# Optimization experiments

Hardware: AMD Instinct MI355X
Metric: run time of the kernel (lower is better)

The kernel has to match this reference:

```python
import jax, jax.numpy as jnp
import numpy as np

EMBED_DIM = 1024
NUM_HEADS = 16
HEAD_DIM = EMBED_DIM // NUM_HEADS
B, T_Q, T_K = 2, 2048, 2048


def setup_inputs() -> dict:
    key = jax.random.key(0)
    ks = jax.random.split(key, 11)
    s = 1.0 / np.sqrt(EMBED_DIM)
    return {
        "query": jax.random.normal(ks[0], (B, T_Q, EMBED_DIM), jnp.float32),
        "key": jax.random.normal(ks[1], (B, T_K, EMBED_DIM), jnp.float32),
        "value": jax.random.normal(ks[2], (B, T_K, EMBED_DIM), jnp.float32),
        "Wq": jax.random.normal(ks[3], (EMBED_DIM, EMBED_DIM), jnp.float32) * s,
        "bq": jnp.zeros((EMBED_DIM,), jnp.float32),
        "Wk": jax.random.normal(ks[4], (EMBED_DIM, EMBED_DIM), jnp.float32) * s,
        "bk": jnp.zeros((EMBED_DIM,), jnp.float32),
        "Wv": jax.random.normal(ks[5], (EMBED_DIM, EMBED_DIM), jnp.float32) * s,
        "bv": jnp.zeros((EMBED_DIM,), jnp.float32),
        "Wo": jax.random.normal(ks[6], (EMBED_DIM, EMBED_DIM), jnp.float32) * s,
        "bo": jnp.zeros((EMBED_DIM,), jnp.float32),
    }


def reference(query, key, value, Wq, bq, Wk, bk, Wv, bv, Wo, bo):
    b, tq, _ = query.shape
    tk = key.shape[1]
    # projections -> [B, H, T, Dh]
    q = (query @ Wq.T + bq).reshape(b, tq, NUM_HEADS, HEAD_DIM).transpose(0, 2, 1, 3)
    k = (key @ Wk.T + bk).reshape(b, tk, NUM_HEADS, HEAD_DIM).transpose(0, 2, 1, 3)
    v = (value @ Wv.T + bv).reshape(b, tk, NUM_HEADS, HEAD_DIM).transpose(0, 2, 1, 3)
    scores = jnp.einsum("bhqd,bhkd->bhqk", q, k) / np.sqrt(HEAD_DIM)
    attn = jax.nn.softmax(scores, axis=-1)
    attn = jnp.nan_to_num(attn, nan=0.0)  # matches torch.nan_to_num; dropout is eval-mode identity
    out = jnp.einsum("bhqk,bhkd->bhqd", attn, v)
    out = out.transpose(0, 2, 1, 3).reshape(b, tq, EMBED_DIM)
    return out @ Wo.T + bo
```

## Files before the change

kernel.cpp:

```cpp
#include <hip/hip_runtime.h>
#include <hip/hip_bf16.h>


typedef short bf16x8 __attribute__((ext_vector_type(8)));
typedef short bf16x4 __attribute__((ext_vector_type(4)));
typedef float f32x4 __attribute__((ext_vector_type(4)));

#define B_ 2
#define T_ 2048
#define E_ 1024
#define H_ 16
#define DH_ 64
#define M_ 4096

static __device__ __forceinline__ short f2bf(float f) {
    __hip_bfloat16 h = __float2bfloat16(f);
    return *reinterpret_cast<short*>(&h);
}

static __device__ __forceinline__ bf16x8 cvt8(const float4 a, const float4 b) {
    bf16x8 r;
    r[0] = f2bf(a.x); r[1] = f2bf(a.y); r[2] = f2bf(a.z); r[3] = f2bf(a.w);
    r[4] = f2bf(b.x); r[5] = f2bf(b.y); r[6] = f2bf(b.z); r[7] = f2bf(b.w);
    return r;
}

static __device__ __forceinline__ void async_copy16(const short* g, short* l) {
    __builtin_amdgcn_global_load_lds(
        (const __attribute__((address_space(1))) unsigned int*)g,
        (__attribute__((address_space(3))) unsigned int*)l, 16, 0, 0);
}

__global__ __launch_bounds__(256) void conv_bf16(
    const float* __restrict__ q, const float* __restrict__ k, const float* __restrict__ v,
    const float* __restrict__ wq, const float* __restrict__ wk,
    const float* __restrict__ wv, const float* __restrict__ wo,
    short* __restrict__ qo, short* __restrict__ ko, short* __restrict__ vo,
    short* __restrict__ wqo, short* __restrict__ wko,
    short* __restrict__ wvo, short* __restrict__ woo) {
    const int y = blockIdx.y;
    const float* src; short* dst; int n;
    switch (y) {
        case 0: src = q;  dst = qo;  n = M_ * E_; break;
        case 1: src = k;  dst = ko;  n = M_ * E_; break;
        case 2: src = v;  dst = vo;  n = M_ * E_; break;
        case 3: src = wq; dst = wqo; n = E_ * E_; break;
        case 4: src = wk; dst = wko; n = E_ * E_; break;
        case 5: src = wv; dst = wvo; n = E_ * E_; break;
        default: src = wo; dst = woo; n = E_ * E_; break;
    }
    const int idx = (blockIdx.x * 256 + threadIdx.x) * 8;
    if (idx >= n) return;
    const float4* p = (const float4*)(src + idx);
    *(bf16x8*)(dst + idx) = cvt8(p[0], p[1]);
}

template <int CMODE>
__device__ __forceinline__ void gemm_fast_tile(const short* __restrict__ A,
                                               const short* __restrict__ W,
                                               const float* __restrict__ bias,
                                               void* __restrict__ C, int bx, int by) {
    __shared__ short Asm[128 * 32];
    __shared__ short Wsm[128 * 32];
    const int tid = threadIdx.x;
    const int wave = tid >> 6, lane = tid & 63, quad = lane >> 4, l16 = lane & 15;
    const int wr = wave >> 1, wc = wave & 1;
    const int m_base = by * 128, n_base = bx * 128;

    const int srow = wave * 32 + (lane >> 2);
    const int scol = (lane & 3) * 8;

    f32x4 acc[4][4] = {};

    for (int k0 = 0; k0 < E_; k0 += 32) {
#pragma unroll
        for (int i = 0; i < 2; i++) {
            async_copy16(&A[(size_t)(m_base + srow + i * 16) * E_ + k0 + scol],
                         &Asm[wave * 1024 + i * 512]);
            async_copy16(&W[(size_t)(n_base + srow + i * 16) * E_ + k0 + scol],
                         &Wsm[wave * 1024 + i * 512]);
        }
        __syncthreads();

        bf16x8 af[4], wf[4];
#pragma unroll
        for (int i = 0; i < 4; i++)
            af[i] = *(const bf16x8*)&Asm[(wr * 64 + i * 16 + l16) * 32 + quad * 8];
#pragma unroll
        for (int j = 0; j < 4; j++)
            wf[j] = *(const bf16x8*)&Wsm[(wc * 64 + j * 16 + l16) * 32 + quad * 8];
#pragma unroll
        for (int i = 0; i < 4; i++)
#pragma unroll
            for (int j = 0; j < 4; j++)
                acc[i][j] = __builtin_amdgcn_mfma_f32_16x16x32_bf16(af[i], wf[j], acc[i][j], 0, 0, 0);
        __syncthreads();
    }

    if (CMODE == 2) {
#pragma unroll
        for (int j = 0; j < 4; j++) {
            const int col = n_base + wc * 64 + j * 16 + l16;
            const float bval = bias[col];
            const int h = col >> 6, d = col & 63;
#pragma unroll
            for (int i = 0; i < 4; i++) {
                const int m0 = m_base + wr * 64 + i * 16 + quad * 4;
                const int b = m0 >> 11, t0 = m0 & 2047;
                bf16x4 v;
#pragma unroll
                for (int r = 0; r < 4; r++) v[r] = f2bf(acc[i][j][r] + bval);
                *(bf16x4*)&((short*)C)[((size_t)(b * H_ + h) * DH_ + d) * T_ + t0] = v;
            }
        }
    } else {
#pragma unroll
        for (int j = 0; j < 4; j++) {
            const int col = n_base + wc * 64 + j * 16 + l16;
            const float bval = bias[col];
#pragma unroll
            for (int i = 0; i < 4; i++)
#pragma unroll
                for (int r = 0; r < 4; r++) {
                    const int m = m_base + wr * 64 + i * 16 + quad * 4 + r;
                    const float v = acc[i][j][r] + bval;
                    if (CMODE == 1) ((float*)C)[(size_t)m * E_ + col] = v;
                    else            ((short*)C)[(size_t)m * E_ + col] = f2bf(v);
                }
        }
    }
}

__global__ __launch_bounds__(256) void qkv_gemm_fast(
    const short* __restrict__ q, const short* __restrict__ k, const short* __restrict__ v,
    const short* __restrict__ Wq, const short* __restrict__ Wk, const short* __restrict__ Wv,
    const float* __restrict__ bq, const float* __restrict__ bk, const float* __restrict__ bv,
    short* __restrict__ Qb, short* __restrict__ Kb, short* __restrict__ Vtb) {
    const int z = blockIdx.z;
    if (z == 0)      gemm_fast_tile<0>(q, Wq, bq, Qb,  blockIdx.x, blockIdx.y);
    else if (z == 1) gemm_fast_tile<0>(k, Wk, bk, Kb,  blockIdx.x, blockIdx.y);
    else             gemm_fast_tile<2>(v, Wv, bv, Vtb, blockIdx.x, blockIdx.y);
}

__global__ __launch_bounds__(256) void o_gemm_fast(const short* __restrict__ A,
                                                   const short* __restrict__ W,
                                                   const float* __restrict__ bias,
                                                   float* __restrict__ C) {
    gemm_fast_tile<1>(A, W, bias, C, blockIdx.x, blockIdx.y);
}

template <int A_BF16, int CMODE>
__device__ __forceinline__ void gemm_tile(const void* __restrict__ A,
                                          const float* __restrict__ W,
                                          const float* __restrict__ bias,
                                          void* __restrict__ C, int bx, int by) {
    __shared__ short Alds[128][40];
    __shared__ short Wlds[128][40];
    const int tid = threadIdx.x;
    const int wave = tid >> 6, lane = tid & 63, quad = lane >> 4, l16 = lane & 15;
    const int wr = wave >> 1, wc = wave & 1;
    const int m_base = by * 128, n_base = bx * 128;
    const int srow = tid >> 1, sch = (tid & 1) * 16;

    f32x4 acc[4][4] = {};

    for (int k0 = 0; k0 < E_; k0 += 32) {
        bf16x8 av0, av1, wv0, wv1;
        if (A_BF16) {
            const short* Ab = (const short*)A;
            av0 = *(const bf16x8*)&Ab[(size_t)(m_base + srow) * E_ + k0 + sch];
            av1 = *(const bf16x8*)&Ab[(size_t)(m_base + srow) * E_ + k0 + sch + 8];
        } else {
            const float4* p = (const float4*)((const float*)A +
                              (size_t)(m_base + srow) * E_ + k0 + sch);
            av0 = cvt8(p[0], p[1]);
            av1 = cvt8(p[2], p[3]);
        }
        {
            const float4* p = (const float4*)(W + (size_t)(n_base + srow) * E_ + k0 + sch);
            wv0 = cvt8(p[0], p[1]);
            wv1 = cvt8(p[2], p[3]);
        }
        *(bf16x8*)&Alds[srow][sch]     = av0;
        *(bf16x8*)&Alds[srow][sch + 8] = av1;
        *(bf16x8*)&Wlds[srow][sch]     = wv0;
        *(bf16x8*)&Wlds[srow][sch + 8] = wv1;
        __syncthreads();

        bf16x8 af[4], bfv[4];
#pragma unroll
        for (int i = 0; i < 4; i++)
            af[i] = *(const bf16x8*)&Alds[wr * 64 + i * 16 + l16][quad * 8];
#pragma unroll
        for (int j = 0; j < 4; j++)
            bfv[j] = *(const bf16x8*)&Wlds[wc * 64 + j * 16 + l16][quad * 8];
#pragma unroll
        for (int i = 0; i < 4; i++)
#pragma unroll
            for (int j = 0; j < 4; j++)
                acc[i][j] = __builtin_amdgcn_mfma_f32_16x16x32_bf16(af[i], bfv[j], acc[i][j], 0, 0, 0);
        __syncthreads();
    }

    if (CMODE == 2) {
#pragma unroll
        for (int j = 0; j < 4; j++) {
            const int col = n_base + wc * 64 + j * 16 + l16;
            const float bval = bias[col];
            const int h = col >> 6, d = col & 63;
#pragma unroll
            for (int i = 0; i < 4; i++) {
                const int m0 = m_base + wr * 64 + i * 16 + quad * 4;
                const int b = m0 >> 11, t0 = m0 & 2047;
                bf16x4 v;
#pragma unroll
                for (int r = 0; r < 4; r++) v[r] = f2bf(acc[i][j][r] + bval);
                *(bf16x4*)&((short*)C)[((size_t)(b * H_ + h) * DH_ + d) * T_ + t0] = v;
            }
        }
    } else {
#pragma unroll
        for (int j = 0; j < 4; j++) {
            const int col = n_base + wc * 64 + j * 16 + l16;
            const float bval = bias[col];
#pragma unroll
            for (int i = 0; i < 4; i++)
#pragma unroll
                for (int r = 0; r < 4; r++) {
                    const int m = m_base + wr * 64 + i * 16 + quad * 4 + r;
                    const float v = acc[i][j][r] + bval;
                    if (CMODE == 1) ((float*)C)[(size_t)m * E_ + col] = v;
                    else            ((short*)C)[(size_t)m * E_ + col] = f2bf(v);
                }
        }
    }
}

__global__ __launch_bounds__(256) void qkv_gemm_slow(
    const float* __restrict__ q, const float* __restrict__ k, const float* __restrict__ v,
    const float* __restrict__ Wq, const float* __restrict__ Wk, const float* __restrict__ Wv,
    const float* __restrict__ bq, const float* __restrict__ bk, const float* __restrict__ bv,
    short* __restrict__ Qb, short* __restrict__ Kb, short* __restrict__ Vtb) {
    const int z = blockIdx.z;
    if (z == 0)      gemm_tile<0, 0>(q, Wq, bq, Qb,  blockIdx.x, blockIdx.y);
    else if (z == 1) gemm_tile<0, 0>(k, Wk, bk, Kb,  blockIdx.x, blockIdx.y);
    else             gemm_tile<0, 2>(v, Wv, bv, Vtb, blockIdx.x, blockIdx.y);
}

__global__ __launch_bounds__(256) void o_gemm_slow(const short* __restrict__ A,
                                                   const float* __restrict__ W,
                                                   const float* __restrict__ bias,
                                                   float* __restrict__ C) {
    gemm_tile<1, 1>(A, W, bias, C, blockIdx.x, blockIdx.y);
}

__global__ __launch_bounds__(256) void attn(short* __restrict__ QO,
                                            const short* __restrict__ Kb,
                                            const short* __restrict__ Vtb) {
    __shared__ short Klds[64][72];
    __shared__ short Vl[64][72];
    __shared__ short Pl[4][16][68];

    const int tid = threadIdx.x;
    const int wave = tid >> 6, lane = tid & 63, quad = lane >> 4, l16 = lane & 15;
    const int bh = blockIdx.x;
    const int b = bh >> 4, h = bh & 15;
    const int q0 = blockIdx.y * 64 + wave * 16;
    const size_t base = ((size_t)b * T_) * E_ + (size_t)h * DH_;
    const size_t vbase = (size_t)bh * DH_ * T_;

    bf16x8 qf[2];
    qf[0] = *(const bf16x8*)&QO[base + (size_t)(q0 + l16) * E_ + quad * 8];
    qf[1] = *(const bf16x8*)&QO[base + (size_t)(q0 + l16) * E_ + 32 + quad * 8];

    f32x4 oacc[4] = {};
    float lsum[4] = {0.f, 0.f, 0.f, 0.f};

    const int srow = tid >> 2;
    const int sc = (tid & 3) * 16;

    for (int kt = 0; kt < T_; kt += 64) {
        const size_t krow = base + (size_t)(kt + srow) * E_;
        *(bf16x8*)&Klds[srow][sc]     = *(const bf16x8*)&Kb[krow + sc];
        *(bf16x8*)&Klds[srow][sc + 8] = *(const bf16x8*)&Kb[krow + sc + 8];
        const size_t vrow = vbase + (size_t)srow * T_ + kt;
        *(bf16x8*)&Vl[srow][sc]     = *(const bf16x8*)&Vtb[vrow + sc];
        *(bf16x8*)&Vl[srow][sc + 8] = *(const bf16x8*)&Vtb[vrow + sc + 8];
        __syncthreads();

        f32x4 sacc[4] = {};
#pragma unroll
        for (int ks = 0; ks < 2; ks++)
#pragma unroll
            for (int kn = 0; kn < 4; kn++) {
                bf16x8 kf = *(const bf16x8*)&Klds[kn * 16 + l16][ks * 32 + quad * 8];
                sacc[kn] = __builtin_amdgcn_mfma_f32_16x16x32_bf16(qf[ks], kf, sacc[kn], 0, 0, 0);
            }

#pragma unroll
        for (int r = 0; r < 4; r++) {
            const float p0 = __expf(sacc[0][r] * 0.125f);
            const float p1 = __expf(sacc[1][r] * 0.125f);
            const float p2 = __expf(sacc[2][r] * 0.125f);
            const float p3 = __expf(sacc[3][r] * 0.125f);
            lsum[r] += (p0 + p1) + (p2 + p3);
            short* prow = &Pl[wave][quad * 4 + r][0];
            prow[l16]      = f2bf(p0);
            prow[16 + l16] = f2bf(p1);
            prow[32 + l16] = f2bf(p2);
            prow[48 + l16] = f2bf(p3);
        }
        __syncthreads();

#pragma unroll
        for (int ks = 0; ks < 2; ks++) {
            bf16x8 pf = *(const bf16x8*)&Pl[wave][l16][ks * 32 + quad * 8];
#pragma unroll
            for (int dn = 0; dn < 4; dn++) {
                bf16x8 vf = *(const bf16x8*)&Vl[dn * 16 + l16][ks * 32 + quad * 8];
                oacc[dn] = __builtin_amdgcn_mfma_f32_16x16x32_bf16(pf, vf, oacc[dn], 0, 0, 0);
            }
        }
        __syncthreads();
    }

#pragma unroll
    for (int r = 0; r < 4; r++) {
#pragma unroll
        for (int m = 1; m < 16; m <<= 1) lsum[r] += __shfl_xor(lsum[r], m);
        lsum[r] = 1.0f / lsum[r];
    }

#pragma unroll
    for (int dn = 0; dn < 4; dn++)
#pragma unroll
        for (int r = 0; r < 4; r++) {
            const float v = oacc[dn][r] * lsum[r];
            QO[base + (size_t)(q0 + quad * 4 + r) * E_ + dn * 16 + l16] = f2bf(v);
        }
}

extern "C" void kernel_launch(void* const* d_in, const int* in_sizes, int n_in,
                              void* d_out, int out_size, void* d_ws, size_t ws_size,
                              hipStream_t stream) {
    const float* query = (const float*)d_in[0];
    const float* key   = (const float*)d_in[1];
    const float* value = (const float*)d_in[2];
    const float* Wq = (const float*)d_in[3];
    const float* bq = (const float*)d_in[4];
    const float* Wk = (const float*)d_in[5];
    const float* bk = (const float*)d_in[6];
    const float* Wv = (const float*)d_in[7];
    const float* bv = (const float*)d_in[8];
    const float* Wo = (const float*)d_in[9];
    const float* bo = (const float*)d_in[10];

    const size_t NE = (size_t)M_ * E_;
    const size_t WE = (size_t)E_ * E_;

    short* Qb  = (short*)d_ws;
    short* Vtb = Qb + NE;
    short* Kb  = (short*)d_out;

    dim3 blk(256);
    const bool fast = ws_size >= (size_t)48 * 1024 * 1024;

    if (fast) {
        short* Qin = Vtb + NE;
        short* Kin = Qin + NE;
        short* Vin = Kin + NE;
        short* Wqb = Vin + NE;
        short* Wkb = Wqb + WE;
        short* Wvb = Wkb + WE;
        short* Wob = Wvb + WE;

        conv_bf16<<<dim3(2048, 7), blk, 0, stream>>>(query, key, value, Wq, Wk, Wv, Wo,
                                                     Qin, Kin, Vin, Wqb, Wkb, Wvb, Wob);
        qkv_gemm_fast<<<dim3(8, 32, 3), blk, 0, stream>>>(Qin, Kin, Vin,
                                                          Wqb, Wkb, Wvb, bq, bk, bv,
                                                          Qb, Kb, Vtb);
        attn<<<dim3(B_ * H_, T_ / 64), blk, 0, stream>>>(Qb, Kb, Vtb);
        o_gemm_fast<<<dim3(8, 32), blk, 0, stream>>>(Qb, Wob, bo, (float*)d_out);
    } else {
        qkv_gemm_slow<<<dim3(8, 32, 3), blk, 0, stream>>>(query, key, value,
                                                          Wq, Wk, Wv, bq, bk, bv,
                                                          Qb, Kb, Vtb);
        attn<<<dim3(B_ * H_, T_ / 64), blk, 0, stream>>>(Qb, Kb, Vtb);
        o_gemm_slow<<<dim3(8, 32), blk, 0, stream>>>(Qb, Wo, bo, (float*)d_out);
    }
}
```

Before: 262.4 us.

## Widen GEMM K-tiles with XOR swizzle, retile O-proj, double-buffer attention

The QKV GEMM now stages 64-wide K slices per barrier and uses an XOR-swizzled LDS layout to reduce bank conflicts. The output projection becomes a standalone 128x64-tile kernel, launched on twice as many blocks. The attention kernel processes 32 query rows per wave and 128 per block, reusing each K/V fragment across two row tiles. It double-buffers K/V in LDS with register prefetch and replaces one barrier with a waitcnt. The aim is to cut barrier count, LDS conflicts and global-load stalls, at the cost of more LDS and registers per block and fewer attention blocks.

```diff
diff --git a/kernel.cpp b/kernel.cpp
--- a/kernel.cpp
+++ b/kernel.cpp
@@ -56,44 +56,54 @@
 }
 
 template <int CMODE>
-__device__ __forceinline__ void gemm_fast_tile(const short* __restrict__ A,
-                                               const short* __restrict__ W,
-                                               const float* __restrict__ bias,
-                                               void* __restrict__ C, int bx, int by) {
-    __shared__ short Asm[128 * 32];
-    __shared__ short Wsm[128 * 32];
+__device__ __forceinline__ void gemm128_tile(const short* __restrict__ A,
+                                             const short* __restrict__ W,
+                                             const float* __restrict__ bias,
+                                             void* __restrict__ C, int bx, int by) {
+    __shared__ short Asm[128 * 64];
+    __shared__ short Wsm[128 * 64];
     const int tid = threadIdx.x;
     const int wave = tid >> 6, lane = tid & 63, quad = lane >> 4, l16 = lane & 15;
     const int wr = wave >> 1, wc = wave & 1;
     const int m_base = by * 128, n_base = bx * 128;
-
-    const int srow = wave * 32 + (lane >> 2);
-    const int scol = (lane & 3) * 8;
+    const int xk = l16 & 7;
+
+    const int srowA = (lane >> 3);
+    const int scc = lane & 7;
 
     f32x4 acc[4][4] = {};
 
-    for (int k0 = 0; k0 < E_; k0 += 32) {
-#pragma unroll
-        for (int i = 0; i < 2; i++) {
-            async_copy16(&A[(size_t)(m_base + srow + i * 16) * E_ + k0 + scol],
-                         &Asm[wave * 1024 + i * 512]);
-            async_copy16(&W[(size_t)(n_base + srow + i * 16) * E_ + k0 + scol],
-                         &Wsm[wave * 1024 + i * 512]);
-        }
-        __syncthreads();
-
-        bf16x8 af[4], wf[4];
-#pragma unroll
-        for (int i = 0; i < 4; i++)
-            af[i] = *(const bf16x8*)&Asm[(wr * 64 + i * 16 + l16) * 32 + quad * 8];
-#pragma unroll
-        for (int j = 0; j < 4; j++)
-            wf[j] = *(const bf16x8*)&Wsm[(wc * 64 + j * 16 + l16) * 32 + quad * 8];
-#pragma unroll
-        for (int i = 0; i < 4; i++)
-#pragma unroll
-            for (int j = 0; j < 4; j++)
-                acc[i][j] = __builtin_amdgcn_mfma_f32_16x16x32_bf16(af[i], wf[j], acc[i][j], 0, 0, 0);
+    for (int k0 = 0; k0 < E_; k0 += 64) {
+#pragma unroll
+        for (int i = 0; i < 4; i++) {
+            const int row = i * 32 + wave * 8 + srowA;
+            const int gc = (scc ^ (row & 7)) * 8;
+            async_copy16(&A[(size_t)(m_base + row) * E_ + k0 + gc],
+                         &Asm[(i * 256 + wave * 64) * 8]);
+            async_copy16(&W[(size_t)(n_base + row) * E_ + k0 + gc],
+                         &Wsm[(i * 256 + wave * 64) * 8]);
+        }
+        __syncthreads();
+
+#pragma unroll
+        for (int ks = 0; ks < 2; ks++) {
+            bf16x8 af[4], wf[4];
+#pragma unroll
+            for (int i = 0; i < 4; i++) {
+                const int rw = wr * 64 + i * 16 + l16;
+                af[i] = *(const bf16x8*)&Asm[rw * 64 + (((ks * 4 + quad) ^ xk) * 8)];
+            }
+#pragma unroll
+            for (int j = 0; j < 4; j++) {
+                const int rw = wc * 64 + j * 16 + l16;
+                wf[j] = *(const bf16x8*)&Wsm[rw * 64 + (((ks * 4 + quad) ^ xk) * 8)];
+            }
+#pragma unroll
+            for (int i = 0; i < 4; i++)
+#pragma unroll
+                for (int j = 0; j < 4; j++)
+                    acc[i][j] = __builtin_amdgcn_mfma_f32_16x16x32_bf16(af[i], wf[j], acc[i][j], 0, 0, 0);
+        }
         __syncthreads();
     }
 
@@ -123,9 +133,7 @@
 #pragma unroll
                 for (int r = 0; r < 4; r++) {
                     const int m = m_base + wr * 64 + i * 16 + quad * 4 + r;
-                    const float v = acc[i][j][r] + bval;
-                    if (CMODE == 1) ((float*)C)[(size_t)m * E_ + col] = v;
-                    else            ((short*)C)[(size_t)m * E_ + col] = f2bf(v);
+                    ((short*)C)[(size_t)m * E_ + col] = f2bf(acc[i][j][r] + bval);
                 }
         }
     }
@@ -137,16 +145,76 @@
     const float* __restrict__ bq, const float* __restrict__ bk, const float* __restrict__ bv,
     short* __restrict__ Qb, short* __restrict__ Kb, short* __restrict__ Vtb) {
     const int z = blockIdx.z;
-    if (z == 0)      gemm_fast_tile<0>(q, Wq, bq, Qb,  blockIdx.x, blockIdx.y);
-    else if (z == 1) gemm_fast_tile<0>(k, Wk, bk, Kb,  blockIdx.x, blockIdx.y);
-    else             gemm_fast_tile<2>(v, Wv, bv, Vtb, blockIdx.x, blockIdx.y);
+    if (z == 0)      gemm128_tile<0>(q, Wq, bq, Qb,  blockIdx.x, blockIdx.y);
+    else if (z == 1) gemm128_tile<0>(k, Wk, bk, Kb,  blockIdx.x, blockIdx.y);
+    else             gemm128_tile<2>(v, Wv, bv, Vtb, blockIdx.x, blockIdx.y);
 }
 
 __global__ __launch_bounds__(256) void o_gemm_fast(const short* __restrict__ A,
                                                    const short* __restrict__ W,
                                                    const float* __restrict__ bias,
                                                    float* __restrict__ C) {
-    gemm_fast_tile<1>(A, W, bias, C, blockIdx.x, blockIdx.y);
+    __shared__ short Asm[128 * 64];
+    __shared__ short Wsm[64 * 64];
+    const int tid = threadIdx.x;
+    const int wave = tid >> 6, lane = tid & 63, quad = lane >> 4, l16 = lane & 15;
+    const int m_base = blockIdx.y * 128, n_base = blockIdx.x * 64;
+    const int xk = l16 & 7;
+    const int srowA = (lane >> 3), scc = lane & 7;
+
+    f32x4 acc[2][4] = {};
+
+    for (int k0 = 0; k0 < E_; k0 += 64) {
+#pragma unroll
+        for (int i = 0; i < 4; i++) {
+            const int row = i * 32 + wave * 8 + srowA;
+            const int gc = (scc ^ (row & 7)) * 8;
+            async_copy16(&A[(size_t)(m_base + row) * E_ + k0 + gc],
+                         &Asm[(i * 256 + wave * 64) * 8]);
+        }
+#pragma unroll
+        for (int i = 0; i < 2; i++) {
+            const int row = i * 32 + wave * 8 + srowA;
+            const int gc = (scc ^ (row & 7)) * 8;
+            async_copy16(&W[(size_t)(n_base + row) * E_ + k0 + gc],
+                         &Wsm[(i * 256 + wave * 64) * 8]);
+        }
+        __syncthreads();
+
+#pragma unroll
+        for (int ks = 0; ks < 2; ks++) {
+            bf16x8 af[2], wf[4];
+#pragma unroll
+            for (int i = 0; i < 2; i++) {
+                const int rw = wave * 32 + i * 16 + l16;
+                af[i] = *(const bf16x8*)&Asm[rw * 64 + (((ks * 4 + quad) ^ xk) * 8)];
+            }
+#pragma unroll
+            for (int j = 0; j < 4; j++) {
+                const int rw = j * 16 + l16;
+                wf[j] = *(const bf16x8*)&Wsm[rw * 64 + (((ks * 4 + quad) ^ xk) * 8)];
+            }
+#pragma unroll
+            for (int i = 0; i < 2; i++)
+#pragma unroll
+                for (int j = 0; j < 4; j++)
+                    acc[i][j] = __builtin_amdgcn_mfma_f32_16x16x32_bf16(af[i], wf[j], acc[i][j], 0, 0, 0);
+        }
+        __syncthreads();
+    }
+
+#pragma unroll
+    for (int j = 0; j < 4; j++) {
+        const int col = n_base + j * 16 + l16;
+        const float bval = bias[col];
+#pragma unroll
+        for (int i = 0; i < 2; i++)
+#pragma unroll
+            for (int r = 0; r < 4; r++) {
+                const int m = m_base + wave * 32 + i * 16 + quad * 4 + r;
+                C[(size_t)m * E_ + col] = acc[i][j][r] + bval;
+            }
+    }
 }
 
 template <int A_BF16, int CMODE>
@@ -257,87 +325,129 @@
 __global__ __launch_bounds__(256) void attn(short* __restrict__ QO,
                                             const short* __restrict__ Kb,
                                             const short* __restrict__ Vtb) {
-    __shared__ short Klds[64][72];
-    __shared__ short Vl[64][72];
-    __shared__ short Pl[4][16][68];
+    __shared__ short Kl[2][64][68];
+    __shared__ short Vl[2][64][68];
+    __shared__ short Pl[4][32][68];
 
     const int tid = threadIdx.x;
     const int wave = tid >> 6, lane = tid & 63, quad = lane >> 4, l16 = lane & 15;
     const int bh = blockIdx.x;
     const int b = bh >> 4, h = bh & 15;
-    const int q0 = blockIdx.y * 64 + wave * 16;
+    const int q0 = blockIdx.y * 128 + wave * 32;
     const size_t base = ((size_t)b * T_) * E_ + (size_t)h * DH_;
     const size_t vbase = (size_t)bh * DH_ * T_;
 
-    bf16x8 qf[2];
-    qf[0] = *(const bf16x8*)&QO[base + (size_t)(q0 + l16) * E_ + quad * 8];
-    qf[1] = *(const bf16x8*)&QO[base + (size_t)(q0 + l16) * E_ + 32 + quad * 8];
-
-    f32x4 oacc[4] = {};
-    float lsum[4] = {0.f, 0.f, 0.f, 0.f};
+    bf16x8 qf[2][2];
+#pragma unroll
+    for (int rt = 0; rt < 2; rt++)
+#pragma unroll
+        for (int ks = 0; ks < 2; ks++)
+            qf[rt][ks] = *(const bf16x8*)&QO[base + (size_t)(q0 + rt * 16 + l16) * E_ + ks * 32 + quad * 8];
+
+    f32x4 oacc[2][4] = {};
+    float lsum[2][4] = {};
 
     const int srow = tid >> 2;
     const int sc = (tid & 3) * 16;
 
-    for (int kt = 0; kt < T_; kt += 64) {
-        const size_t krow = base + (size_t)(kt + srow) * E_;
-        *(bf16x8*)&Klds[srow][sc]     = *(const bf16x8*)&Kb[krow + sc];
-        *(bf16x8*)&Klds[srow][sc + 8] = *(const bf16x8*)&Kb[krow + sc + 8];
-        const size_t vrow = vbase + (size_t)srow * T_ + kt;
-        *(bf16x8*)&Vl[srow][sc]     = *(const bf16x8*)&Vtb[vrow + sc];
-        *(bf16x8*)&Vl[srow][sc + 8] = *(const bf16x8*)&Vtb[vrow + sc + 8];
-        __syncthreads();
-
-        f32x4 sacc[4] = {};
-#pragma unroll
-        for (int ks = 0; ks < 2; ks++)
-#pragma unroll
-            for (int kn = 0; kn < 4; kn++) {
-                bf16x8 kf = *(const bf16x8*)&Klds[kn * 16 + l16][ks * 32 + quad * 8];
-                sacc[kn] = __builtin_amdgcn_mfma_f32_16x16x32_bf16(qf[ks], kf, sacc[kn], 0, 0, 0);
-            }
-
+    {
+        const size_t krow = base + (size_t)srow * E_;
+        *(bf16x8*)&Kl[0][srow][sc]     = *(const bf16x8*)&Kb[krow + sc];
+        *(bf16x8*)&Kl[0][srow][sc + 8] = *(const bf16x8*)&Kb[krow + sc + 8];
+        const size_t vrow = vbase + (size_t)srow * T_;
+        *(bf16x8*)&Vl[0][srow][sc]     = *(const bf16x8*)&Vtb[vrow + sc];
+        *(bf16x8*)&Vl[0][srow][sc + 8] = *(const bf16x8*)&Vtb[vrow + sc + 8];
+    }
+    __syncthreads();
+
+    for (int it = 0; it < T_ / 64; it++) {
+        const int cur = it & 1;
+        const bool have = (it + 1) < T_ / 64;
+
+        bf16x8 nk0, nk1, nv0, nv1;
+        if (have) {
+            const int kt = (it + 1) * 64;
+            const size_t krow = base + (size_t)(kt + srow) * E_;
+            nk0 = *(const bf16x8*)&Kb[krow + sc];
+            nk1 = *(const bf16x8*)&Kb[krow + sc + 8];
+            const size_t vrow = vbase + (size_t)srow * T_ + kt;
+            nv0 = *(const bf16x8*)&Vtb[vrow + sc];
+            nv1 = *(const bf16x8*)&Vtb[vrow + sc + 8];
+        }
+
+        f32x4 sacc[2][4] = {};
+#pragma unroll
+        for (int ks = 0; ks < 2; ks++) {
+            bf16x8 kf[4];
+#pragma unroll
+            for (int kn = 0; kn < 4; kn++)
+                kf[kn] = *(const bf16x8*)&Kl[cur][kn * 16 + l16][ks * 32 + quad * 8];
+#pragma unroll
+            for (int rt = 0; rt < 2; rt++)
+#pragma unroll
+                for (int kn = 0; kn < 4; kn++)
+                    sacc[rt][kn] = __builtin_amdgcn_mfma_f32_16x16x32_bf16(qf[rt][ks], kf[kn], sacc[rt][kn], 0, 0, 0);
+        }
+
+#pragma unroll
+        for (int rt = 0; rt < 2; rt++)
+#pragma unroll
+            for (int r = 0; r < 4; r++) {
+                const float p0 = __expf(sacc[rt][0][r] * 0.125f);
+                const float p1 = __expf(sacc[rt][1][r] * 0.125f);
+                const float p2 = __expf(sacc[rt][2][r] * 0.125f);
+                const float p3 = __expf(sacc[rt][3][r] * 0.125f);
+                lsum[rt][r] += (p0 + p1) + (p2 + p3);
+                short* prow = &Pl[wave][rt * 16 + quad * 4 + r][0];
+                prow[l16]      = f2bf(p0);
+                prow[16 + l16] = f2bf(p1);
+                prow[32 + l16] = f2bf(p2);
+                prow[48 + l16] = f2bf(p3);
+            }
+        asm volatile("s_waitcnt lgkmcnt(0)" ::: "memory");
+
+#pragma unroll
+        for (int ks = 0; ks < 2; ks++) {
+            bf16x8 pf[2];
+#pragma unroll
+            for (int rt = 0; rt < 2; rt++)
+                pf[rt] = *(const bf16x8*)&Pl[wave][rt * 16 + l16][ks * 32 + quad * 8];
+#pragma unroll
+            for (int dn = 0; dn < 4; dn++) {
+                bf16x8 vf = *(const bf16x8*)&Vl[cur][dn * 16 + l16][ks * 32 + quad * 8];
+#pragma unroll
+                for (int rt = 0; rt < 2; rt++)
+                    oacc[rt][dn] = __builtin_amdgcn_mfma_f32_16x16x32_bf16(pf[rt], vf, oacc[rt][dn], 0, 0, 0);
+            }
+        }
+
+        if (have) {
+            *(bf16x8*)&Kl[cur ^ 1][srow][sc]     = nk0;
+            *(bf16x8*)&Kl[cur ^ 1][srow][sc + 8] = nk1;
+            *(bf16x8*)&Vl[cur ^ 1][srow][sc]     = nv0;
+            *(bf16x8*)&Vl[cur ^ 1][srow][sc + 8] = nv1;
+        }
+        __syncthreads();
+    }
+
+#pragma unroll
+    for (int rt = 0; rt < 2; rt++)
 #pragma unroll
         for (int r = 0; r < 4; r++) {
-            const float p0 = __expf(sacc[0][r] * 0.125f);
-            const float p1 = __expf(sacc[1][r] * 0.125f);
-            const float p2 = __expf(sacc[2][r] * 0.125f);
-            const float p3 = __expf(sacc[3][r] * 0.125f);
-            lsum[r] += (p0 + p1) + (p2 + p3);
-            short* prow = &Pl[wave][quad * 4 + r][0];
-            prow[l16]      = f2bf(p0);
-            prow[16 + l16] = f2bf(p1);
-            prow[32 + l16] = f2bf(p2);
-            prow[48 + l16] = f2bf(p3);
-        }
-        __syncthreads();
-
-#pragma unroll
-        for (int ks = 0; ks < 2; ks++) {
-            bf16x8 pf = *(const bf16x8*)&Pl[wave][l16][ks * 32 + quad * 8];
-#pragma unroll
-            for (int dn = 0; dn < 4; dn++) {
-                bf16x8 vf = *(const bf16x8*)&Vl[dn * 16 + l16][ks * 32 + quad * 8];
-                oacc[dn] = __builtin_amdgcn_mfma_f32_16x16x32_bf16(pf, vf, oacc[dn], 0, 0, 0);
-            }
-        }
-        __syncthreads();
-    }
-
-#pragma unroll
-    for (int r = 0; r < 4; r++) {
-#pragma unroll
-        for (int m = 1; m < 16; m <<= 1) lsum[r] += __shfl_xor(lsum[r], m);
-        lsum[r] = 1.0f / lsum[r];
-    }
-
-#pragma unroll
-    for (int dn = 0; dn < 4; dn++)
-#pragma unroll
-        for (int r = 0; r < 4; r++) {
-            const float v = oacc[dn][r] * lsum[r];
-            QO[base + (size_t)(q0 + quad * 4 + r) * E_ + dn * 16 + l16] = f2bf(v);
-        }
+#pragma unroll
+            for (int m = 1; m < 16; m <<= 1) lsum[rt][r] += __shfl_xor(lsum[rt][r], m);
+            lsum[rt][r] = 1.0f / lsum[rt][r];
+        }
+
+#pragma unroll
+    for (int rt = 0; rt < 2; rt++)
+#pragma unroll
+        for (int dn = 0; dn < 4; dn++)
+#pragma unroll
+            for (int r = 0; r < 4; r++) {
+                const float v = oacc[rt][dn][r] * lsum[rt][r];
+                QO[base + (size_t)(q0 + rt * 16 + quad * 4 + r) * E_ + dn * 16 + l16] = f2bf(v);
+            }
 }
 
 extern "C" void kernel_launch(void* const* d_in, const int* in_sizes, int n_in,
@@ -379,13 +489,13 @@
         qkv_gemm_fast<<<dim3(8, 32, 3), blk, 0, stream>>>(Qin, Kin, Vin,
                                                           Wqb, Wkb, Wvb, bq, bk, bv,
                                                           Qb, Kb, Vtb);
-        attn<<<dim3(B_ * H_, T_ / 64), blk, 0, stream>>>(Qb, Kb, Vtb);
-        o_gemm_fast<<<dim3(8, 32), blk, 0, stream>>>(Qb, Wob, bo, (float*)d_out);
+        attn<<<dim3(B_ * H_, T_ / 128), blk, 0, stream>>>(Qb, Kb, Vtb);
+        o_gemm_fast<<<dim3(16, 32), blk, 0, stream>>>(Qb, Wob, bo, (float*)d_out);
     } else {
         qkv_gemm_slow<<<dim3(8, 32, 3), blk, 0, stream>>>(query, key, value,
                                                           Wq, Wk, Wv, bq, bk, bv,
                                                           Qb, Kb, Vtb);
-        attn<<<dim3(B_ * H_, T_ / 64), blk, 0, stream>>>(Qb, Kb, Vtb);
+        attn<<<dim3(B_ * H_, T_ / 128), blk, 0, stream>>>(Qb, Kb, Vtb);
         o_gemm_slow<<<dim3(8, 32), blk, 0, stream>>>(Qb, Wo, bo, (float*)d_out);
     }
 }
```

After: 245.5 us. -6.4%, faster.
